# Performance work log

Hardware: AMD Instinct MI355X
Metric: run time of the kernel (lower is better)

Reference implementation:

```python
import jax, jax.numpy as jnp
import numpy as np

NUM_HEADS = 16
HEAD_DIM = 64
ROPE_THETA = 10000.0


def _rope_cos_sin(n, dtype):
    # Llama RoPE: inv_freq over even dims, emb = concat(freqs, freqs)
    inv_freq = 1.0 / (ROPE_THETA ** (jnp.arange(0, HEAD_DIM, 2, dtype=jnp.float32) / HEAD_DIM))
    freqs = jnp.arange(n, dtype=jnp.float32)[:, None] * inv_freq[None, :]  # [N, D/2]
    emb = jnp.concatenate([freqs, freqs], axis=-1)  # [N, D]
    return jnp.cos(emb).astype(dtype), jnp.sin(emb).astype(dtype)


def _rotate_half(x):
    x1, x2 = jnp.split(x, 2, axis=-1)
    return jnp.concatenate([-x2, x1], axis=-1)


def setup_inputs() -> dict:
    key = jax.random.key(0)
    ks = jax.random.split(key, 5)
    B, N, H = 2, 2048, 1024
    feature = jax.random.normal(ks[0], (B, N, H), dtype=jnp.float32)
    attention_mask = jnp.ones((B, N), dtype=jnp.int32)
    scale = 0.02
    Wq = jax.random.normal(ks[1], (H, H), dtype=jnp.float32) * scale
    Wk = jax.random.normal(ks[2], (H, H), dtype=jnp.float32) * scale
    Wv = jax.random.normal(ks[3], (H, H), dtype=jnp.float32) * scale
    Wo = jax.random.normal(ks[4], (H, H), dtype=jnp.float32) * scale
    return {"feature": feature, "attention_mask": attention_mask,
            "Wq": Wq, "Wk": Wk, "Wv": Wv, "Wo": Wo}


def reference(feature, attention_mask, Wq, Wk, Wv, Wo):
    B, N, H = feature.shape
    h, d = NUM_HEADS, HEAD_DIM
    scale = d ** -0.5

    def proj(x, W):  # nn.Linear(bias=False): x @ W.T
        y = jnp.einsum('bnh,oh->bno', x, W)
        return y.reshape(B, N, h, d).transpose(0, 2, 1, 3)  # [B,h,N,d]

    q, k, v = proj(feature, Wq), proj(feature, Wk), proj(feature, Wv)

    cos, sin = _rope_cos_sin(N, feature.dtype)  # [N, d]
    cos = cos[None, None]  # [1,1,N,d]
    sin = sin[None, None]
    q = q * cos + _rotate_half(q) * sin
    k = k * cos + _rotate_half(k) * sin

    scores = jnp.einsum('bhqd,bhkd->bhqk', q, k) * scale  # [B,h,N,N]
    mask = (attention_mask != 0)[:, None, None, :]  # [B,1,1,N]
    scores = jnp.where(mask, scores, jnp.float32(-jnp.inf).astype(scores.dtype))
    weights = jax.nn.softmax(scores, axis=-1)

    out = jnp.einsum('bhqk,bhkd->bhqd', weights, v)  # [B,h,N,d]
    out = out.transpose(0, 2, 1, 3).reshape(B, N, H)
    return jnp.einsum('bnh,oh->bno', out, Wo)
```

## Files before the change

kernel.cpp:

```cpp
#include <hip/hip_runtime.h>
#include <hip/hip_bf16.h>

typedef __attribute__((ext_vector_type(4))) float f32x4;
typedef __attribute__((ext_vector_type(8))) short s16x8;
typedef __attribute__((ext_vector_type(4))) short s16x4;

#define BB 2
#define NN 2048
#define HH 1024
#define NHEAD 16
#define HDIM 64

__device__ __forceinline__ short f2bf(float f) {
  union { float f; unsigned u; } v; v.f = f;
  unsigned r = v.u + 0x7fffu + ((v.u >> 16) & 1u);
  return (short)(r >> 16);
}

__device__ __forceinline__ f32x4 zf4() { f32x4 z; z[0]=0.f; z[1]=0.f; z[2]=0.f; z[3]=0.f; return z; }

__device__ __forceinline__ f32x4 mfma16(s16x8 a, s16x8 b, f32x4 c) {
  return __builtin_amdgcn_mfma_f32_16x16x32_bf16(a, b, c, 0, 0, 0);
}

__device__ __forceinline__ s16x4 cvt4(f32x4 v) {
  s16x4 o; o[0]=f2bf(v[0]); o[1]=f2bf(v[1]); o[2]=f2bf(v[2]); o[3]=f2bf(v[3]); return o;
}

__device__ __forceinline__ float vexp2(float x) {
  float r; asm("v_exp_f32 %0, %1" : "=v"(r) : "v"(x)); return r;
}

__device__ __forceinline__ float vrcp(float x) {
  float r; asm("v_rcp_f32 %0, %1" : "=v"(r) : "v"(x)); return r;
}

__device__ __forceinline__ float vmax3(float a, float b, float c) {
  float r; asm("v_max3_f32 %0, %1, %2, %3" : "=v"(r) : "v"(a), "v"(b), "v"(c)); return r;
}

__device__ __forceinline__ unsigned cvtpk_bf16(float lo, float hi) {
  unsigned r; asm("v_cvt_pk_bf16_f32 %0, %1, %2" : "=v"(r) : "v"(lo), "v"(hi)); return r;
}

__device__ __forceinline__ void gload_lds16(const short* g, short* l) {
  __builtin_amdgcn_global_load_lds(
      (const __attribute__((address_space(1))) unsigned*)g,
      (__attribute__((address_space(3))) unsigned*)l, 16, 0, 0);
}

__global__ __launch_bounds__(256) void prep_kernel(
    const float* __restrict__ feat, const int* __restrict__ mask,
    const float* __restrict__ wq, const float* __restrict__ wk,
    const float* __restrict__ wv, const float* __restrict__ wo,
    short* __restrict__ fbf, short* __restrict__ wqb, short* __restrict__ wkb,
    short* __restrict__ wvb, short* __restrict__ wob,
    float* __restrict__ cosb, float* __restrict__ sinb,
    float* __restrict__ mbias, int* __restrict__ mseg) {
  const int tid = blockIdx.x * blockDim.x + threadIdx.x;
  const int nth = gridDim.x * blockDim.x;
  const int NF4 = BB*NN*HH/4;
  for (int i = tid; i < NF4; i += nth)
    ((s16x4*)fbf)[i] = cvt4(((const f32x4*)feat)[i]);
  const int NW4 = HH*HH/4;
  for (int i = tid; i < NW4; i += nth) {
    ((s16x4*)wqb)[i] = cvt4(((const f32x4*)wq)[i]);
    ((s16x4*)wkb)[i] = cvt4(((const f32x4*)wk)[i]);
    ((s16x4*)wvb)[i] = cvt4(((const f32x4*)wv)[i]);
    ((s16x4*)wob)[i] = cvt4(((const f32x4*)wo)[i]);
  }
  for (int i = tid; i < NN*32; i += nth) {
    int pos = i >> 5, f = i & 31;
    float inv = __expf(-(float)f * 0.28782313662425572f);
    float ang = (float)pos * inv;
    float s, c;
    sincosf(ang, &s, &c);
    cosb[i] = c; sinb[i] = s;
  }
  for (int i = tid; i < BB*NN; i += nth)
    mbias[i] = mask[i] ? 0.f : -1.0e30f;
  for (int i = tid; i < BB*(NN/64); i += nth) {
    int bb = i / (NN/64), sg = i % (NN/64);
    int any = 0;
    for (int j = 0; j < 64; ++j) any |= (mask[bb*NN + sg*64 + j] == 0);
    mseg[i] = any;
  }
}

__device__ __forceinline__ void gemm128_core(
    const short* __restrict__ A, const short* __restrict__ W,
    int bm, int bn, short* smem, f32x4 acc[4][4]) {
  const int tid = threadIdx.x;
  const int lane = tid & 63, wid = tid >> 6;
  const int wr = wid >> 1, wc = wid & 1;
  const int g = lane >> 4, lr = lane & 15;
#pragma unroll
  for (int i = 0; i < 4; ++i)
#pragma unroll
    for (int j = 0; j < 4; ++j) acc[i][j] = zf4();

  const int srow = wid*16 + (lane >> 2);
  const int scol = (lane & 3) * 8;
  const short* Abase = A + (size_t)(bm*128 + srow)*HH + scol;
  const short* Wbase = W + (size_t)(bn*128 + srow)*HH + scol;

  auto stage = [&](int b, int t) {
    const short* ga = Abase + t*32;
    const short* gb = Wbase + t*32;
    short* la = smem + b*8192 + wid*512;
    short* lb = smem + b*8192 + 4096 + wid*512;
    gload_lds16(ga,          la);
    gload_lds16(ga + 64*HH,  la + 2048);
    gload_lds16(gb,          lb);
    gload_lds16(gb + 64*HH,  lb + 2048);
  };

  stage(0, 0);
  asm volatile("s_waitcnt vmcnt(0)");
  __syncthreads();

  const int NT = HH / 32;
  int cur = 0;
  for (int t = 0; t < NT; ++t) {
    if (t + 1 < NT) stage(cur ^ 1, t + 1);
    const short* At = smem + cur*8192;
    const short* Bt = At + 4096;
    s16x8 af[4], bf[4];
#pragma unroll
    for (int mf = 0; mf < 4; ++mf)
      af[mf] = *(const s16x8*)&At[(wr*64 + mf*16 + lr)*32 + g*8];
#pragma unroll
    for (int nf = 0; nf < 4; ++nf)
      bf[nf] = *(const s16x8*)&Bt[(wc*64 + nf*16 + lr)*32 + g*8];
#pragma unroll
    for (int mf = 0; mf < 4; ++mf)
#pragma unroll
      for (int nf = 0; nf < 4; ++nf)
        acc[mf][nf] = mfma16(af[mf], bf[nf], acc[mf][nf]);
    __syncthreads();
    cur ^= 1;
  }
}

__global__ __launch_bounds__(256) void qkv_kernel(
    const short* __restrict__ fbf, const short* __restrict__ wqb,
    const short* __restrict__ wkb, const short* __restrict__ wvb,
    const float* __restrict__ cosb, const float* __restrict__ sinb,
    short* __restrict__ qb, short* __restrict__ kb, short* __restrict__ vtb) {
  __shared__ short smem[18432];
  const int bm = blockIdx.y, bn = blockIdx.x, z = blockIdx.z;
  const short* W = (z == 0) ? wqb : ((z == 1) ? wkb : wvb);
  f32x4 acc[4][4];
  gemm128_core(fbf, W, bm, bn, smem, acc);

  const int tid = threadIdx.x, lane = tid & 63, wid = tid >> 6;
  const int wr = wid >> 1, wc = wid & 1, g = lane >> 4, lr = lane & 15;
  const int head = bn*2 + wc;
  const int m0 = bm*128 + wr*64;
  const int b = m0 / NN;

  if (z < 2) {
    short* dst = (z == 0) ? qb : kb;
    const float scale = (z == 0) ? 0.18033688011112042f : 1.0f;
#pragma unroll
    for (int mf = 0; mf < 4; ++mf) {
#pragma unroll
      for (int r = 0; r < 4; ++r) {
        int m = m0 + mf*16 + g*4 + r;
        int n = m & (NN - 1);
        float c0 = cosb[n*32 + lr],      s0 = sinb[n*32 + lr];
        float c1 = cosb[n*32 + 16 + lr], s1 = sinb[n*32 + 16 + lr];
        float v0 = acc[mf][0][r], v1 = acc[mf][1][r];
        float v2 = acc[mf][2][r], v3 = acc[mf][3][r];
        float o0 = (v0*c0 - v2*s0) * scale;
        float o1 = (v1*c1 - v3*s1) * scale;
        float o2 = (v2*c0 + v0*s0) * scale;
        float o3 = (v3*c1 + v1*s1) * scale;
        size_t base = ((size_t)(b*NHEAD + head)*NN + n)*HDIM;
        dst[base +  0 + lr] = f2bf(o0);
        dst[base + 16 + lr] = f2bf(o1);
        dst[base + 32 + lr] = f2bf(o2);
        dst[base + 48 + lr] = f2bf(o3);
      }
    }
  } else {
    __syncthreads();
    short* tp = smem + wid*4608;
#pragma unroll
    for (int mf = 0; mf < 4; ++mf)
#pragma unroll
      for (int nf = 0; nf < 4; ++nf)
#pragma unroll
        for (int r = 0; r < 4; ++r)
          tp[(nf*16 + lr)*72 + mf*16 + g*4 + r] = f2bf(acc[mf][nf][r]);
    __syncthreads();
    const int nbase = m0 & (NN - 1);
    size_t vbase = ((size_t)(b*NHEAD + head)*HDIM)*NN;
#pragma unroll
    for (int it = 0; it < 8; ++it) {
      int j  = it*8 + (lane >> 3);
      int ns = (lane & 7)*8;
      s16x8 vv = *(const s16x8*)&tp[j*72 + ns];
      *(s16x8*)&vtb[vbase + (size_t)j*NN + nbase + ns] = vv;
    }
  }
}

__global__ __launch_bounds__(256) void attn_kernel(
    const short* __restrict__ qb, const short* __restrict__ kb,
    const short* __restrict__ vtb, const float* __restrict__ mbias,
    const int* __restrict__ mseg,
    short* __restrict__ attnb) {
  __shared__ short Kt[2][64*72];
  __shared__ short Vt[2][64*72];
  const int tid = threadIdx.x, lane = tid & 63, wid = tid >> 6;
  const int g = lane >> 4, lr = lane & 15;
  const int bh = blockIdx.y; const int b = bh >> 4;
  const int q0 = blockIdx.x*64 + wid*16;

  const short* qp = qb + ((size_t)bh*NN + q0 + lr)*HDIM + g*8;
  s16x8 qf0 = *(const s16x8*)(qp);
  s16x8 qf1 = *(const s16x8*)(qp + 32);

  s16x8 one8;
#pragma unroll
  for (int i = 0; i < 8; ++i) one8[i] = (short)0x3F80;

  f32x4 acc[4];
#pragma unroll
  for (int i = 0; i < 4; ++i) acc[i] = zf4();
  f32x4 accl = zf4();
  float mrun = -3.0e38f;

  const int* msp = mseg + b*(NN/64);
  int segflag = (lane < 32) ? msp[lane] : 0;
  unsigned segbits = (unsigned)__ballot(segflag != 0);

  const int sr = tid >> 2;
  const int sc = (tid & 3) * 16;
  const int rK = ((sr >> 5) & 1)*32 + ((sr >> 2) & 1)*16 + ((sr >> 3) & 3)*4 + (sr & 3);
  const short* kp = kb + (size_t)bh*NN*HDIM + (size_t)sr*HDIM + sc;
  const short* vp = vtb + ((size_t)bh*HDIM + sr)*NN + sc;
  const float* mb = mbias + b*NN;

  s16x8 kr0 = *(const s16x8*)(kp);
  s16x8 kr1 = *(const s16x8*)(kp + 8);
  s16x8 vr0 = *(const s16x8*)(vp);
  s16x8 vr1 = *(const s16x8*)(vp + 8);
  *(s16x8*)&Kt[0][rK*72 + sc]     = kr0;
  *(s16x8*)&Kt[0][rK*72 + sc + 8] = kr1;
  *(s16x8*)&Vt[0][sr*72 + sc]     = vr0;
  *(s16x8*)&Vt[0][sr*72 + sc + 8] = vr1;
  __syncthreads();

  int cur = 0;
  for (int k0 = 0; k0 < NN; k0 += 64) {
    const bool nl = (k0 + 64 < NN);
    if (nl) {
      kp += 64*HDIM; vp += 64;
      kr0 = *(const s16x8*)(kp);
      kr1 = *(const s16x8*)(kp + 8);
      vr0 = *(const s16x8*)(vp);
      vr1 = *(const s16x8*)(vp + 8);
    }
    const short* KtC = Kt[cur];
    const short* VtC = Vt[cur];

    f32x4 s[4];
    __builtin_amdgcn_s_setprio(1);
#pragma unroll
    for (int j = 0; j < 4; ++j) {
      s16x8 ka0 = *(const s16x8*)&KtC[(j*16 + lr)*72 + g*8];
      s16x8 ka1 = *(const s16x8*)&KtC[(j*16 + lr)*72 + 32 + g*8];
      s[j] = mfma16(ka1, qf1, mfma16(ka0, qf0, zf4()));
    }
    __builtin_amdgcn_s_setprio(0);

    if (segbits & (1u << (k0 >> 6))) {
#pragma unroll
      for (int j = 0; j < 4; ++j) {
        f32x4 bi = *(const f32x4*)&mb[k0 + (j >> 1)*32 + (j & 1)*4 + g*8];
#pragma unroll
        for (int r = 0; r < 4; ++r) s[j][r] += bi[r];
      }
    }

    float t0 = vmax3(s[0][0], s[0][1], s[0][2]);
    float t1 = vmax3(s[0][3], s[1][0], s[1][1]);
    float t2 = vmax3(s[1][2], s[1][3], s[2][0]);
    float t3 = vmax3(s[2][1], s[2][2], s[2][3]);
    float t4 = vmax3(s[3][0], s[3][1], s[3][2]);
    float lmax = fmaxf(vmax3(t0, t1, t2), vmax3(t3, t4, s[3][3]));

    if (__any(lmax > mrun + 8.f)) {
      float rmax = fmaxf(lmax, __shfl_xor(lmax, 16));
      rmax = fmaxf(rmax, __shfl_xor(rmax, 32));
      float mnew = fmaxf(mrun, rmax);
      float al = vexp2(mrun - mnew);
      mrun = mnew;
      float alr[4];
#pragma unroll
      for (int r = 0; r < 4; ++r)
        alr[r] = __shfl(al, (lane & 48) | (g*4 + r));
#pragma unroll
      for (int r = 0; r < 4; ++r) {
        acc[0][r] *= alr[r]; acc[1][r] *= alr[r];
        acc[2][r] *= alr[r]; acc[3][r] *= alr[r];
        accl[r]   *= alr[r];
      }
    }

    float p[4][4];
#pragma unroll
    for (int j = 0; j < 4; ++j) {
      p[j][0] = vexp2(s[j][0] - mrun);
      p[j][1] = vexp2(s[j][1] - mrun);
      p[j][2] = vexp2(s[j][2] - mrun);
      p[j][3] = vexp2(s[j][3] - mrun);
    }
    union { unsigned u[4]; s16x8 v; } A0, A1;
    A0.u[0] = cvtpk_bf16(p[0][0], p[0][1]);
    A0.u[1] = cvtpk_bf16(p[0][2], p[0][3]);
    A0.u[2] = cvtpk_bf16(p[1][0], p[1][1]);
    A0.u[3] = cvtpk_bf16(p[1][2], p[1][3]);
    A1.u[0] = cvtpk_bf16(p[2][0], p[2][1]);
    A1.u[1] = cvtpk_bf16(p[2][2], p[2][3]);
    A1.u[2] = cvtpk_bf16(p[3][0], p[3][1]);
    A1.u[3] = cvtpk_bf16(p[3][2], p[3][3]);

    __builtin_amdgcn_s_setprio(1);
    accl = mfma16(A0.v, one8, accl);
    accl = mfma16(A1.v, one8, accl);
#pragma unroll
    for (int db = 0; db < 4; ++db) {
      s16x8 vb0 = *(const s16x8*)&VtC[(db*16 + lr)*72 + g*8];
      s16x8 vb1 = *(const s16x8*)&VtC[(db*16 + lr)*72 + 32 + g*8];
      acc[db] = mfma16(A0.v, vb0, acc[db]);
      acc[db] = mfma16(A1.v, vb1, acc[db]);
    }
    __builtin_amdgcn_s_setprio(0);

    if (nl) {
      *(s16x8*)&Kt[cur^1][rK*72 + sc]     = kr0;
      *(s16x8*)&Kt[cur^1][rK*72 + sc + 8] = kr1;
      *(s16x8*)&Vt[cur^1][sr*72 + sc]     = vr0;
      *(s16x8*)&Vt[cur^1][sr*72 + sc + 8] = vr1;
      __syncthreads();
      cur ^= 1;
    }
  }

#pragma unroll
  for (int r = 0; r < 4; ++r) {
    float inv = vrcp(accl[r]);
    size_t row = (size_t)(b*NN + q0 + g*4 + r);
#pragma unroll
    for (int db = 0; db < 4; ++db)
      attnb[row*HH + (bh & 15)*64 + db*16 + lr] = f2bf(acc[db][r]*inv);
  }
}

__global__ __launch_bounds__(256) void outproj_kernel(
    const short* __restrict__ attnb, const short* __restrict__ wob,
    float* __restrict__ out) {
  __shared__ short smem[16384];
  const int bm = blockIdx.y, bn = blockIdx.x;
  f32x4 acc[4][4];
  gemm128_core(attnb, wob, bm, bn, smem, acc);
  const int tid = threadIdx.x, lane = tid & 63, wid = tid >> 6;
  const int wr = wid >> 1, wc = wid & 1, g = lane >> 4, lr = lane & 15;
  const int m0 = bm*128 + wr*64;
  const int c0 = bn*128 + wc*64;
#pragma unroll
  for (int mf = 0; mf < 4; ++mf)
#pragma unroll
    for (int r = 0; r < 4; ++r) {
      int m = m0 + mf*16 + g*4 + r;
      float* po = out + (size_t)m*HH + c0;
#pragma unroll
      for (int nf = 0; nf < 4; ++nf)
        po[nf*16 + lr] = acc[mf][nf][r];
    }
}

extern "C" void kernel_launch(void* const* d_in, const int* in_sizes, int n_in,
                              void* d_out, int out_size, void* d_ws, size_t ws_size,
                              hipStream_t stream) {
  const float* feat = (const float*)d_in[0];
  const int*   mask = (const int*)d_in[1];
  const float* wq   = (const float*)d_in[2];
  const float* wk   = (const float*)d_in[3];
  const float* wv   = (const float*)d_in[4];
  const float* wo   = (const float*)d_in[5];
  float* out = (float*)d_out;

  char* ws = (char*)d_ws;
  size_t off = 0;
  short* fbf = (short*)(ws + off); off += (size_t)BB*NN*HH*2;
  short* wqb = (short*)(ws + off); off += (size_t)HH*HH*2;
  short* wkb = (short*)(ws + off); off += (size_t)HH*HH*2;
  short* wvb = (short*)(ws + off); off += (size_t)HH*HH*2;
  short* wob = (short*)(ws + off); off += (size_t)HH*HH*2;
  float* cosb = (float*)(ws + off); off += (size_t)NN*32*4;
  float* sinb = (float*)(ws + off); off += (size_t)NN*32*4;
  float* mbias = (float*)(ws + off); off += (size_t)BB*NN*4;
  int* msegb = (int*)(ws + off); off += (size_t)BB*(NN/64)*4;
  short* qbuf = (short*)(ws + off); off += (size_t)BB*NN*HH*2;
  short* kbuf = (short*)(ws + off); off += (size_t)BB*NN*HH*2;
  short* vtbuf = (short*)(ws + off); off += (size_t)BB*NN*HH*2;
  short* attnb = (short*)(ws + off); off += (size_t)BB*NN*HH*2;

  prep_kernel<<<1024, 256, 0, stream>>>(feat, mask, wq, wk, wv, wo,
                                        fbf, wqb, wkb, wvb, wob, cosb, sinb,
                                        mbias, msegb);
  qkv_kernel<<<dim3(HH/128, BB*NN/128, 3), 256, 0, stream>>>(
      fbf, wqb, wkb, wvb, cosb, sinb, qbuf, kbuf, vtbuf);
  attn_kernel<<<dim3(NN/64, BB*NHEAD), 256, 0, stream>>>(
      qbuf, kbuf, vtbuf, mbias, msegb, attnb);
  outproj_kernel<<<dim3(HH/128, BB*NN/128), 256, 0, stream>>>(attnb, wob, out);
}
```

Measured before the change: 126.4 us.

## Process two 16-row query tiles per wave in attention kernel

```diff
diff --git a/kernel.cpp b/kernel.cpp
--- a/kernel.cpp
+++ b/kernel.cpp
@@ -216,21 +216,24 @@
   const int tid = threadIdx.x, lane = tid & 63, wid = tid >> 6;
   const int g = lane >> 4, lr = lane & 15;
   const int bh = blockIdx.y; const int b = bh >> 4;
-  const int q0 = blockIdx.x*64 + wid*16;
-
-  const short* qp = qb + ((size_t)bh*NN + q0 + lr)*HDIM + g*8;
-  s16x8 qf0 = *(const s16x8*)(qp);
-  s16x8 qf1 = *(const s16x8*)(qp + 32);
+  const int q0 = blockIdx.x*128 + wid*32;
+
+  const short* qpA = qb + ((size_t)bh*NN + q0 + lr)*HDIM + g*8;
+  s16x8 qfA0 = *(const s16x8*)(qpA);
+  s16x8 qfA1 = *(const s16x8*)(qpA + 32);
+  const short* qpB = qpA + 16*HDIM;
+  s16x8 qfB0 = *(const s16x8*)(qpB);
+  s16x8 qfB1 = *(const s16x8*)(qpB + 32);
 
   s16x8 one8;
 #pragma unroll
   for (int i = 0; i < 8; ++i) one8[i] = (short)0x3F80;
 
-  f32x4 acc[4];
-#pragma unroll
-  for (int i = 0; i < 4; ++i) acc[i] = zf4();
-  f32x4 accl = zf4();
-  float mrun = -3.0e38f;
+  f32x4 accA[4], accB[4];
+#pragma unroll
+  for (int i = 0; i < 4; ++i) { accA[i] = zf4(); accB[i] = zf4(); }
+  f32x4 acclA = zf4(), acclB = zf4();
+  float mrunA = -3.0e38f, mrunB = -3.0e38f;
 
   const int* msp = mseg + b*(NN/64);
   int segflag = (lane < 32) ? msp[lane] : 0;
@@ -266,13 +269,14 @@
     const short* KtC = Kt[cur];
     const short* VtC = Vt[cur];
 
-    f32x4 s[4];
+    f32x4 sA[4], sB[4];
     __builtin_amdgcn_s_setprio(1);
 #pragma unroll
     for (int j = 0; j < 4; ++j) {
       s16x8 ka0 = *(const s16x8*)&KtC[(j*16 + lr)*72 + g*8];
       s16x8 ka1 = *(const s16x8*)&KtC[(j*16 + lr)*72 + 32 + g*8];
-      s[j] = mfma16(ka1, qf1, mfma16(ka0, qf0, zf4()));
+      sA[j] = mfma16(ka1, qfA1, mfma16(ka0, qfA0, zf4()));
+      sB[j] = mfma16(ka1, qfB1, mfma16(ka0, qfB0, zf4()));
     }
     __builtin_amdgcn_s_setprio(0);
 
@@ -281,62 +285,109 @@
       for (int j = 0; j < 4; ++j) {
         f32x4 bi = *(const f32x4*)&mb[k0 + (j >> 1)*32 + (j & 1)*4 + g*8];
 #pragma unroll
-        for (int r = 0; r < 4; ++r) s[j][r] += bi[r];
-      }
-    }
-
-    float t0 = vmax3(s[0][0], s[0][1], s[0][2]);
-    float t1 = vmax3(s[0][3], s[1][0], s[1][1]);
-    float t2 = vmax3(s[1][2], s[1][3], s[2][0]);
-    float t3 = vmax3(s[2][1], s[2][2], s[2][3]);
-    float t4 = vmax3(s[3][0], s[3][1], s[3][2]);
-    float lmax = fmaxf(vmax3(t0, t1, t2), vmax3(t3, t4, s[3][3]));
-
-    if (__any(lmax > mrun + 8.f)) {
-      float rmax = fmaxf(lmax, __shfl_xor(lmax, 16));
+        for (int r = 0; r < 4; ++r) { sA[j][r] += bi[r]; sB[j][r] += bi[r]; }
+      }
+    }
+
+    float a0 = vmax3(sA[0][0], sA[0][1], sA[0][2]);
+    float a1 = vmax3(sA[0][3], sA[1][0], sA[1][1]);
+    float a2 = vmax3(sA[1][2], sA[1][3], sA[2][0]);
+    float a3 = vmax3(sA[2][1], sA[2][2], sA[2][3]);
+    float a4 = vmax3(sA[3][0], sA[3][1], sA[3][2]);
+    float lmaxA = fmaxf(vmax3(a0, a1, a2), vmax3(a3, a4, sA[3][3]));
+    float b0 = vmax3(sB[0][0], sB[0][1], sB[0][2]);
+    float b1 = vmax3(sB[0][3], sB[1][0], sB[1][1]);
+    float b2 = vmax3(sB[1][2], sB[1][3], sB[2][0]);
+    float b3 = vmax3(sB[2][1], sB[2][2], sB[2][3]);
+    float b4 = vmax3(sB[3][0], sB[3][1], sB[3][2]);
+    float lmaxB = fmaxf(vmax3(b0, b1, b2), vmax3(b3, b4, sB[3][3]));
+
+    if (__any(lmaxA > mrunA + 8.f)) {
+      float rmax = fmaxf(lmaxA, __shfl_xor(lmaxA, 16));
       rmax = fmaxf(rmax, __shfl_xor(rmax, 32));
-      float mnew = fmaxf(mrun, rmax);
-      float al = vexp2(mrun - mnew);
-      mrun = mnew;
+      float mnew = fmaxf(mrunA, rmax);
+      float al = vexp2(mrunA - mnew);
+      mrunA = mnew;
       float alr[4];
 #pragma unroll
       for (int r = 0; r < 4; ++r)
         alr[r] = __shfl(al, (lane & 48) | (g*4 + r));
 #pragma unroll
       for (int r = 0; r < 4; ++r) {
-        acc[0][r] *= alr[r]; acc[1][r] *= alr[r];
-        acc[2][r] *= alr[r]; acc[3][r] *= alr[r];
-        accl[r]   *= alr[r];
-      }
-    }
-
-    float p[4][4];
-#pragma unroll
-    for (int j = 0; j < 4; ++j) {
-      p[j][0] = vexp2(s[j][0] - mrun);
-      p[j][1] = vexp2(s[j][1] - mrun);
-      p[j][2] = vexp2(s[j][2] - mrun);
-      p[j][3] = vexp2(s[j][3] - mrun);
-    }
-    union { unsigned u[4]; s16x8 v; } A0, A1;
-    A0.u[0] = cvtpk_bf16(p[0][0], p[0][1]);
-    A0.u[1] = cvtpk_bf16(p[0][2], p[0][3]);
-    A0.u[2] = cvtpk_bf16(p[1][0], p[1][1]);
-    A0.u[3] = cvtpk_bf16(p[1][2], p[1][3]);
-    A1.u[0] = cvtpk_bf16(p[2][0], p[2][1]);
-    A1.u[1] = cvtpk_bf16(p[2][2], p[2][3]);
-    A1.u[2] = cvtpk_bf16(p[3][0], p[3][1]);
-    A1.u[3] = cvtpk_bf16(p[3][2], p[3][3]);
+        accA[0][r] *= alr[r]; accA[1][r] *= alr[r];
+        accA[2][r] *= alr[r]; accA[3][r] *= alr[r];
+        acclA[r]   *= alr[r];
+      }
+    }
+    if (__any(lmaxB > mrunB + 8.f)) {
+      float rmax = fmaxf(lmaxB, __shfl_xor(lmaxB, 16));
+      rmax = fmaxf(rmax, __shfl_xor(rmax, 32));
+      float mnew = fmaxf(mrunB, rmax);
+      float al = vexp2(mrunB - mnew);
+      mrunB = mnew;
+      float alr[4];
+#pragma unroll
+      for (int r = 0; r < 4; ++r)
+        alr[r] = __shfl(al, (lane & 48) | (g*4 + r));
+#pragma unroll
+      for (int r = 0; r < 4; ++r) {
+        accB[0][r] *= alr[r]; accB[1][r] *= alr[r];
+        accB[2][r] *= alr[r]; accB[3][r] *= alr[r];
+        acclB[r]   *= alr[r];
+      }
+    }
+
+    union { unsigned u[4]; s16x8 v; } A0, A1, B0, B1;
+    {
+      float p[4][4];
+#pragma unroll
+      for (int j = 0; j < 4; ++j) {
+        p[j][0] = vexp2(sA[j][0] - mrunA);
+        p[j][1] = vexp2(sA[j][1] - mrunA);
+        p[j][2] = vexp2(sA[j][2] - mrunA);
+        p[j][3] = vexp2(sA[j][3] - mrunA);
+      }
+      A0.u[0] = cvtpk_bf16(p[0][0], p[0][1]);
+      A0.u[1] = cvtpk_bf16(p[0][2], p[0][3]);
+      A0.u[2] = cvtpk_bf16(p[1][0], p[1][1]);
+      A0.u[3] = cvtpk_bf16(p[1][2], p[1][3]);
+      A1.u[0] = cvtpk_bf16(p[2][0], p[2][1]);
+      A1.u[1] = cvtpk_bf16(p[2][2], p[2][3]);
+      A1.u[2] = cvtpk_bf16(p[3][0], p[3][1]);
+      A1.u[3] = cvtpk_bf16(p[3][2], p[3][3]);
+    }
+    {
+      float p[4][4];
+#pragma unroll
+      for (int j = 0; j < 4; ++j) {
+        p[j][0] = vexp2(sB[j][0] - mrunB);
+        p[j][1] = vexp2(sB[j][1] - mrunB);
+        p[j][2] = vexp2(sB[j][2] - mrunB);
+        p[j][3] = vexp2(sB[j][3] - mrunB);
+      }
+      B0.u[0] = cvtpk_bf16(p[0][0], p[0][1]);
+      B0.u[1] = cvtpk_bf16(p[0][2], p[0][3]);
+      B0.u[2] = cvtpk_bf16(p[1][0], p[1][1]);
+      B0.u[3] = cvtpk_bf16(p[1][2], p[1][3]);
+      B1.u[0] = cvtpk_bf16(p[2][0], p[2][1]);
+      B1.u[1] = cvtpk_bf16(p[2][2], p[2][3]);
+      B1.u[2] = cvtpk_bf16(p[3][0], p[3][1]);
+      B1.u[3] = cvtpk_bf16(p[3][2], p[3][3]);
+    }
 
     __builtin_amdgcn_s_setprio(1);
-    accl = mfma16(A0.v, one8, accl);
-    accl = mfma16(A1.v, one8, accl);
+    acclA = mfma16(A0.v, one8, acclA);
+    acclA = mfma16(A1.v, one8, acclA);
+    acclB = mfma16(B0.v, one8, acclB);
+    acclB = mfma16(B1.v, one8, acclB);
 #pragma unroll
     for (int db = 0; db < 4; ++db) {
       s16x8 vb0 = *(const s16x8*)&VtC[(db*16 + lr)*72 + g*8];
       s16x8 vb1 = *(const s16x8*)&VtC[(db*16 + lr)*72 + 32 + g*8];
-      acc[db] = mfma16(A0.v, vb0, acc[db]);
-      acc[db] = mfma16(A1.v, vb1, acc[db]);
+      accA[db] = mfma16(A0.v, vb0, accA[db]);
+      accA[db] = mfma16(A1.v, vb1, accA[db]);
+      accB[db] = mfma16(B0.v, vb0, accB[db]);
+      accB[db] = mfma16(B1.v, vb1, accB[db]);
     }
     __builtin_amdgcn_s_setprio(0);
 
@@ -352,11 +403,15 @@
 
 #pragma unroll
   for (int r = 0; r < 4; ++r) {
-    float inv = vrcp(accl[r]);
-    size_t row = (size_t)(b*NN + q0 + g*4 + r);
-#pragma unroll
-    for (int db = 0; db < 4; ++db)
-      attnb[row*HH + (bh & 15)*64 + db*16 + lr] = f2bf(acc[db][r]*inv);
+    float invA = vrcp(acclA[r]);
+    float invB = vrcp(acclB[r]);
+    size_t rowA = (size_t)(b*NN + q0 + g*4 + r);
+    size_t rowB = rowA + 16;
+#pragma unroll
+    for (int db = 0; db < 4; ++db) {
+      attnb[rowA*HH + (bh & 15)*64 + db*16 + lr] = f2bf(accA[db][r]*invA);
+      attnb[rowB*HH + (bh & 15)*64 + db*16 + lr] = f2bf(accB[db][r]*invB);
+    }
   }
 }
 
@@ -415,7 +470,7 @@
                                         mbias, msegb);
   qkv_kernel<<<dim3(HH/128, BB*NN/128, 3), 256, 0, stream>>>(
       fbf, wqb, wkb, wvb, cosb, sinb, qbuf, kbuf, vtbuf);
-  attn_kernel<<<dim3(NN/64, BB*NHEAD), 256, 0, stream>>>(
+  attn_kernel<<<dim3(NN/128, BB*NHEAD), 256, 0, stream>>>(
       qbuf, kbuf, vtbuf, mbias, msegb, attnb);
   outproj_kernel<<<dim3(HH/128, BB*NN/128), 256, 0, stream>>>(attnb, wob, out);
 }
```

Result: faster. 121.2 us (-4.1%).

## Process 64 query rows per wave in attention to reuse K/V tiles

Applied to the files above, without the earlier changes.

```diff
diff --git a/kernel.cpp b/kernel.cpp
--- a/kernel.cpp
+++ b/kernel.cpp
@@ -206,7 +206,7 @@
   }
 }
 
-__global__ __launch_bounds__(256) void attn_kernel(
+__global__ __launch_bounds__(256, 1) void attn_kernel(
     const short* __restrict__ qb, const short* __restrict__ kb,
     const short* __restrict__ vtb, const float* __restrict__ mbias,
     const int* __restrict__ mseg,
@@ -215,22 +215,35 @@
   __shared__ short Vt[2][64*72];
   const int tid = threadIdx.x, lane = tid & 63, wid = tid >> 6;
   const int g = lane >> 4, lr = lane & 15;
-  const int bh = blockIdx.y; const int b = bh >> 4;
-  const int q0 = blockIdx.x*64 + wid*16;
-
-  const short* qp = qb + ((size_t)bh*NN + q0 + lr)*HDIM + g*8;
-  s16x8 qf0 = *(const s16x8*)(qp);
-  s16x8 qf1 = *(const s16x8*)(qp + 32);
+  const int w = blockIdx.x;
+  const int bh = (w & 7)*4 + ((w >> 3) & 3);
+  const int qt = w >> 5;
+  const int b = bh >> 4;
+  const int q0 = qt*256 + wid*64;
+
+  s16x8 qf[4][2];
+#pragma unroll
+  for (int grp = 0; grp < 4; ++grp) {
+    const short* qp = qb + ((size_t)bh*NN + q0 + grp*16 + lr)*HDIM + g*8;
+    qf[grp][0] = *(const s16x8*)(qp);
+    qf[grp][1] = *(const s16x8*)(qp + 32);
+  }
 
   s16x8 one8;
 #pragma unroll
   for (int i = 0; i < 8; ++i) one8[i] = (short)0x3F80;
 
-  f32x4 acc[4];
-#pragma unroll
-  for (int i = 0; i < 4; ++i) acc[i] = zf4();
-  f32x4 accl = zf4();
-  float mrun = -3.0e38f;
+  f32x4 acc[4][4];
+#pragma unroll
+  for (int i = 0; i < 4; ++i)
+#pragma unroll
+    for (int j = 0; j < 4; ++j) acc[i][j] = zf4();
+  f32x4 accl[4];
+#pragma unroll
+  for (int i = 0; i < 4; ++i) accl[i] = zf4();
+  float mrun[4];
+#pragma unroll
+  for (int i = 0; i < 4; ++i) mrun[i] = -3.0e38f;
 
   const int* msp = mseg + b*(NN/64);
   int segflag = (lane < 32) ? msp[lane] : 0;
@@ -266,13 +279,15 @@
     const short* KtC = Kt[cur];
     const short* VtC = Vt[cur];
 
-    f32x4 s[4];
+    f32x4 s[4][4];
     __builtin_amdgcn_s_setprio(1);
 #pragma unroll
     for (int j = 0; j < 4; ++j) {
       s16x8 ka0 = *(const s16x8*)&KtC[(j*16 + lr)*72 + g*8];
       s16x8 ka1 = *(const s16x8*)&KtC[(j*16 + lr)*72 + 32 + g*8];
-      s[j] = mfma16(ka1, qf1, mfma16(ka0, qf0, zf4()));
+#pragma unroll
+      for (int grp = 0; grp < 4; ++grp)
+        s[grp][j] = mfma16(ka1, qf[grp][1], mfma16(ka0, qf[grp][0], zf4()));
     }
     __builtin_amdgcn_s_setprio(0);
 
@@ -281,62 +296,76 @@
       for (int j = 0; j < 4; ++j) {
         f32x4 bi = *(const f32x4*)&mb[k0 + (j >> 1)*32 + (j & 1)*4 + g*8];
 #pragma unroll
-        for (int r = 0; r < 4; ++r) s[j][r] += bi[r];
+        for (int grp = 0; grp < 4; ++grp)
+#pragma unroll
+          for (int r = 0; r < 4; ++r) s[grp][j][r] += bi[r];
       }
     }
 
-    float t0 = vmax3(s[0][0], s[0][1], s[0][2]);
-    float t1 = vmax3(s[0][3], s[1][0], s[1][1]);
-    float t2 = vmax3(s[1][2], s[1][3], s[2][0]);
-    float t3 = vmax3(s[2][1], s[2][2], s[2][3]);
-    float t4 = vmax3(s[3][0], s[3][1], s[3][2]);
-    float lmax = fmaxf(vmax3(t0, t1, t2), vmax3(t3, t4, s[3][3]));
-
-    if (__any(lmax > mrun + 8.f)) {
-      float rmax = fmaxf(lmax, __shfl_xor(lmax, 16));
-      rmax = fmaxf(rmax, __shfl_xor(rmax, 32));
-      float mnew = fmaxf(mrun, rmax);
-      float al = vexp2(mrun - mnew);
-      mrun = mnew;
-      float alr[4];
-#pragma unroll
-      for (int r = 0; r < 4; ++r)
-        alr[r] = __shfl(al, (lane & 48) | (g*4 + r));
-#pragma unroll
-      for (int r = 0; r < 4; ++r) {
-        acc[0][r] *= alr[r]; acc[1][r] *= alr[r];
-        acc[2][r] *= alr[r]; acc[3][r] *= alr[r];
-        accl[r]   *= alr[r];
+    s16x8 pa[4][2];
+#pragma unroll
+    for (int grp = 0; grp < 4; ++grp) {
+      float t0 = vmax3(s[grp][0][0], s[grp][0][1], s[grp][0][2]);
+      float t1 = vmax3(s[grp][0][3], s[grp][1][0], s[grp][1][1]);
+      float t2 = vmax3(s[grp][1][2], s[grp][1][3], s[grp][2][0]);
+      float t3 = vmax3(s[grp][2][1], s[grp][2][2], s[grp][2][3]);
+      float t4 = vmax3(s[grp][3][0], s[grp][3][1], s[grp][3][2]);
+      float lmax = fmaxf(vmax3(t0, t1, t2), vmax3(t3, t4, s[grp][3][3]));
+
+      if (__any(lmax > mrun[grp] + 8.f)) {
+        float rmax = fmaxf(lmax, __shfl_xor(lmax, 16));
+        rmax = fmaxf(rmax, __shfl_xor(rmax, 32));
+        float mnew = fmaxf(mrun[grp], rmax);
+        float al = vexp2(mrun[grp] - mnew);
+        mrun[grp] = mnew;
+        float alr[4];
+#pragma unroll
+        for (int r = 0; r < 4; ++r)
+          alr[r] = __shfl(al, (lane & 48) | (g*4 + r));
+#pragma unroll
+        for (int r = 0; r < 4; ++r) {
+          acc[grp][0][r] *= alr[r]; acc[grp][1][r] *= alr[r];
+          acc[grp][2][r] *= alr[r]; acc[grp][3][r] *= alr[r];
+          accl[grp][r]   *= alr[r];
+        }
       }
-    }
-
-    float p[4][4];
-#pragma unroll
-    for (int j = 0; j < 4; ++j) {
-      p[j][0] = vexp2(s[j][0] - mrun);
-      p[j][1] = vexp2(s[j][1] - mrun);
-      p[j][2] = vexp2(s[j][2] - mrun);
-      p[j][3] = vexp2(s[j][3] - mrun);
-    }
-    union { unsigned u[4]; s16x8 v; } A0, A1;
-    A0.u[0] = cvtpk_bf16(p[0][0], p[0][1]);
-    A0.u[1] = cvtpk_bf16(p[0][2], p[0][3]);
-    A0.u[2] = cvtpk_bf16(p[1][0], p[1][1]);
-    A0.u[3] = cvtpk_bf16(p[1][2], p[1][3]);
-    A1.u[0] = cvtpk_bf16(p[2][0], p[2][1]);
-    A1.u[1] = cvtpk_bf16(p[2][2], p[2][3]);
-    A1.u[2] = cvtpk_bf16(p[3][0], p[3][1]);
-    A1.u[3] = cvtpk_bf16(p[3][2], p[3][3]);
+
+      float p[4][4];
+#pragma unroll
+      for (int j = 0; j < 4; ++j) {
+        p[j][0] = vexp2(s[grp][j][0] - mrun[grp]);
+        p[j][1] = vexp2(s[grp][j][1] - mrun[grp]);
+        p[j][2] = vexp2(s[grp][j][2] - mrun[grp]);
+        p[j][3] = vexp2(s[grp][j][3] - mrun[grp]);
+      }
+      union { unsigned u[4]; s16x8 v; } P0, P1;
+      P0.u[0] = cvtpk_bf16(p[0][0], p[0][1]);
+      P0.u[1] = cvtpk_bf16(p[0][2], p[0][3]);
+      P0.u[2] = cvtpk_bf16(p[1][0], p[1][1]);
+      P0.u[3] = cvtpk_bf16(p[1][2], p[1][3]);
+      P1.u[0] = cvtpk_bf16(p[2][0], p[2][1]);
+      P1.u[1] = cvtpk_bf16(p[2][2], p[2][3]);
+      P1.u[2] = cvtpk_bf16(p[3][0], p[3][1]);
+      P1.u[3] = cvtpk_bf16(p[3][2], p[3][3]);
+      pa[grp][0] = P0.v;
+      pa[grp][1] = P1.v;
+    }
 
     __builtin_amdgcn_s_setprio(1);
-    accl = mfma16(A0.v, one8, accl);
-    accl = mfma16(A1.v, one8, accl);
+#pragma unroll
+    for (int grp = 0; grp < 4; ++grp) {
+      accl[grp] = mfma16(pa[grp][0], one8, accl[grp]);
+      accl[grp] = mfma16(pa[grp][1], one8, accl[grp]);
+    }
 #pragma unroll
     for (int db = 0; db < 4; ++db) {
       s16x8 vb0 = *(const s16x8*)&VtC[(db*16 + lr)*72 + g*8];
       s16x8 vb1 = *(const s16x8*)&VtC[(db*16 + lr)*72 + 32 + g*8];
-      acc[db] = mfma16(A0.v, vb0, acc[db]);
-      acc[db] = mfma16(A1.v, vb1, acc[db]);
+#pragma unroll
+      for (int grp = 0; grp < 4; ++grp) {
+        acc[grp][db] = mfma16(pa[grp][0], vb0, acc[grp][db]);
+        acc[grp][db] = mfma16(pa[grp][1], vb1, acc[grp][db]);
+      }
     }
     __builtin_amdgcn_s_setprio(0);
 
@@ -351,12 +380,15 @@
   }
 
 #pragma unroll
-  for (int r = 0; r < 4; ++r) {
-    float inv = vrcp(accl[r]);
-    size_t row = (size_t)(b*NN + q0 + g*4 + r);
-#pragma unroll
-    for (int db = 0; db < 4; ++db)
-      attnb[row*HH + (bh & 15)*64 + db*16 + lr] = f2bf(acc[db][r]*inv);
+  for (int grp = 0; grp < 4; ++grp) {
+#pragma unroll
+    for (int r = 0; r < 4; ++r) {
+      float inv = vrcp(accl[grp][r]);
+      size_t row = (size_t)(b*NN + q0 + grp*16 + g*4 + r);
+#pragma unroll
+      for (int db = 0; db < 4; ++db)
+        attnb[row*HH + (bh & 15)*64 + db*16 + lr] = f2bf(acc[grp][db][r]*inv);
+    }
   }
 }
 
@@ -415,7 +447,7 @@
                                         mbias, msegb);
   qkv_kernel<<<dim3(HH/128, BB*NN/128, 3), 256, 0, stream>>>(
       fbf, wqb, wkb, wvb, cosb, sinb, qbuf, kbuf, vtbuf);
-  attn_kernel<<<dim3(NN/64, BB*NHEAD), 256, 0, stream>>>(
+  attn_kernel<<<256, 256, 0, stream>>>(
       qbuf, kbuf, vtbuf, mbias, msegb, attnb);
   outproj_kernel<<<dim3(HH/128, BB*NN/128), 256, 0, stream>>>(attnb, wob, out);
 }
```

After: 129.1 us. 2.2% more time.
